# Kernel optimization log

Hardware: AMD Instinct MI355X
Metric: run time of the kernel (lower is better)

The kernel has to match this reference:

```python
import jax, jax.numpy as jnp
import numpy as np

B, T, H, W = 1024, 10, 32, 32
D = H * W          # MoE token dim = image_width**2
HID = 2 * D        # MoE expert hidden size
E, K = 4, 1        # num_experts, top_k
N_MOE = 5          # transform, add, quad, cubic, fourth


def setup_inputs() -> dict:
    key = jax.random.key(0)
    ks = jax.random.split(key, 6)
    s = 0.02
    return {
        "input": jax.random.normal(ks[0], (B, T, 1, H, W), jnp.float32),
        "conv1_w": jax.random.normal(ks[1], (10, 1, 3, 3, 3), jnp.float32) * s,
        "conv1_b": jnp.zeros((10,), jnp.float32),
        "conv2_w": jax.random.normal(ks[2], (1, 10, T, 3, 3), jnp.float32) * s,
        "conv2_b": jnp.zeros((1,), jnp.float32),
        "w_gate": jax.random.normal(ks[3], (N_MOE, D, E), jnp.float32) * s,
        "w1": jax.random.normal(ks[4], (N_MOE, E, D, HID), jnp.float32) * s,
        "b1": jnp.zeros((N_MOE, E, HID), jnp.float32),
        "w2": jax.random.normal(ks[5], (N_MOE, E, HID, D), jnp.float32) * s,
        "b2": jnp.zeros((N_MOE, E, D), jnp.float32),
    }


def _conv3d(x, w, b, pad):
    y = jax.lax.conv_general_dilated(
        x, w, (1, 1, 1), pad, dimension_numbers=("NCDHW", "OIDHW", "NCDHW"))
    return y + b[None, :, None, None, None]


def _cv_squared(x):
    eps = 1e-10
    return jnp.var(x, ddof=1) / (jnp.mean(x) ** 2 + eps)


def _moe(tok, wg, w1, b1, w2, b2):
    # tok: (B, D). Eval-mode noisy-top-k gating (clean logits, no noise).
    logits = tok @ wg                                   # (B, E)
    top_vals, top_idx = jax.lax.top_k(logits, K)
    top_g = jax.nn.softmax(top_vals, axis=1)            # k=1 -> gate == 1.0
    gates = jnp.zeros_like(logits).at[
        jnp.arange(tok.shape[0])[:, None], top_idx].set(top_g)
    # dense all-expert MLP (E=4 is small), combined by sparse gates
    h = jax.nn.relu(jnp.einsum("bd,edh->beh", tok, w1) + b1)
    y = jnp.einsum("beh,ehd->bed", h, w2) + b2
    out = jnp.einsum("be,bed->bd", gates, y)
    importance = gates.sum(0)
    load = (gates > 0).astype(tok.dtype).sum(0)
    loss = (_cv_squared(importance) + _cv_squared(load)) * 1e-2
    return out, loss


def reference(input, conv1_w, conv1_b, conv2_w, conv2_b, w_gate, w1, b1, w2, b2):
    x = jnp.transpose(input, (0, 2, 1, 3, 4))           # (B,1,T,H,W)
    x = jax.nn.relu(_conv3d(x, conv1_w, conv1_b, [(1, 1), (1, 1), (1, 1)]))
    x = jax.nn.relu(_conv3d(x, conv2_w, conv2_b, [(0, 0), (1, 1), (1, 1)]))  # (B,1,1,H,W)
    tok = x.reshape(x.shape[0], -1)                     # (B, D)
    outs, losses = jax.vmap(_moe, in_axes=(None, 0, 0, 0, 0, 0))(
        tok, w_gate, w1, b1, w2, b2)                    # (5,B,D), (5,)
    f = outs.reshape(N_MOE, -1, 1, 1, H, W)             # each broadcasts over T
    transform, add, quad, cubic, fourth = f[0], f[1], f[2], f[3], f[4]
    i2 = input * input
    poly = (i2 * i2 * fourth + i2 * input * cubic + i2 * quad
            + input * transform + add)
    out = jax.nn.sigmoid(poly)                          # encoder/decoder = identity
    return out, jnp.sum(losses)
```

## Files before the change

### kernel.cpp

```cpp
#include <hip/hip_runtime.h>
#include <hip/hip_bf16.h>


typedef __bf16 bf16x8 __attribute__((ext_vector_type(8)));
typedef __bf16 bf16x4 __attribute__((ext_vector_type(4)));
typedef __bf16 bf16x2 __attribute__((ext_vector_type(2)));
typedef float f32x4 __attribute__((ext_vector_type(4)));

#define NMOE 5
#define NEXP 4

__global__ __launch_bounds__(256, 3) void conv_tok_kernel(
    const float* __restrict__ input, const float* __restrict__ c1w,
    const float* __restrict__ c1b, const float* __restrict__ c2w,
    const float* __restrict__ c2b, float* __restrict__ tok_f32,
    __bf16* __restrict__ tok_bf16)
{
    __shared__ float in_s[10][34][34];
    __shared__ float P[34][34];
    const int b = blockIdx.x, tid = threadIdx.x;

    float* ls = &in_s[0][0][0];
    for (int i = tid; i < 10 * 34 * 34; i += 256) ls[i] = 0.f;
    for (int i = tid; i < 34 * 34; i += 256) (&P[0][0])[i] = 0.f;
    __syncthreads();

    const float* ip = input + (size_t)b * 10240;
    for (int i = tid; i < 2560; i += 256) {
        int t = i >> 8, rem = i & 255;
        int h = rem >> 3, w4 = rem & 7;
        float4 v = ((const float4*)ip)[i];
        float* dst = &in_s[t][h + 1][w4 * 4 + 1];
        dst[0] = v.x; dst[1] = v.y; dst[2] = v.z; dst[3] = v.w;
    }
    __syncthreads();

    const int wcol = tid & 31;
    const int r0 = (tid >> 5) * 4;
    const float c2bias = c2b[0];
    float tk0 = c2bias, tk1 = c2bias, tk2 = c2bias, tk3 = c2bias;

    for (int c = 0; c < 10; ++c) {
        float w1l[27];
        #pragma unroll
        for (int i = 0; i < 27; ++i) w1l[i] = c1w[c * 27 + i];
        const float c1bias = c1b[c];

        float a0[10], a1[10], a2[10], a3[10];
        #pragma unroll
        for (int t = 0; t < 10; ++t) {
            a0[t] = c1bias; a1[t] = c1bias; a2[t] = c1bias; a3[t] = c1bias;
        }

        #pragma unroll
        for (int ts = 0; ts < 10; ++ts) {
            float p0[3], p1[3], p2[3], p3[3], p4[3], p5[3];
            #pragma unroll
            for (int dw = 0; dw < 3; ++dw) {
                p0[dw] = in_s[ts][r0 + 0][wcol + dw];
                p1[dw] = in_s[ts][r0 + 1][wcol + dw];
                p2[dw] = in_s[ts][r0 + 2][wcol + dw];
                p3[dw] = in_s[ts][r0 + 3][wcol + dw];
                p4[dw] = in_s[ts][r0 + 4][wcol + dw];
                p5[dw] = in_s[ts][r0 + 5][wcol + dw];
            }
            #pragma unroll
            for (int dt = 0; dt < 3; ++dt) {
                const int t = ts - dt + 1;
                if (t < 0 || t > 9) continue;
                #pragma unroll
                for (int dw = 0; dw < 3; ++dw) {
                    float u0 = w1l[dt * 9 + 0 + dw];
                    float u1 = w1l[dt * 9 + 3 + dw];
                    float u2 = w1l[dt * 9 + 6 + dw];
                    a0[t] += u0 * p0[dw] + u1 * p1[dw] + u2 * p2[dw];
                    a1[t] += u0 * p1[dw] + u1 * p2[dw] + u2 * p3[dw];
                    a2[t] += u0 * p2[dw] + u1 * p3[dw] + u2 * p4[dw];
                    a3[t] += u0 * p3[dw] + u1 * p4[dw] + u2 * p5[dw];
                }
            }
            if (ts >= 1) {
                const int td = ts - 1;
                __syncthreads();
                P[r0 + 1][wcol + 1] = fmaxf(a0[td], 0.f);
                P[r0 + 2][wcol + 1] = fmaxf(a1[td], 0.f);
                P[r0 + 3][wcol + 1] = fmaxf(a2[td], 0.f);
                P[r0 + 4][wcol + 1] = fmaxf(a3[td], 0.f);
                __syncthreads();
                const int wb = (c * 10 + td) * 9;
                #pragma unroll
                for (int dw = 0; dw < 3; ++dw) {
                    float q0 = P[r0 + 0][wcol + dw];
                    float q1 = P[r0 + 1][wcol + dw];
                    float q2 = P[r0 + 2][wcol + dw];
                    float q3 = P[r0 + 3][wcol + dw];
                    float q4 = P[r0 + 4][wcol + dw];
                    float q5 = P[r0 + 5][wcol + dw];
                    float u0 = c2w[wb + 0 + dw];
                    float u1 = c2w[wb + 3 + dw];
                    float u2 = c2w[wb + 6 + dw];
                    tk0 += u0 * q0 + u1 * q1 + u2 * q2;
                    tk1 += u0 * q1 + u1 * q2 + u2 * q3;
                    tk2 += u0 * q2 + u1 * q3 + u2 * q4;
                    tk3 += u0 * q3 + u1 * q4 + u2 * q5;
                }
            }
        }
        {
            __syncthreads();
            P[r0 + 1][wcol + 1] = fmaxf(a0[9], 0.f);
            P[r0 + 2][wcol + 1] = fmaxf(a1[9], 0.f);
            P[r0 + 3][wcol + 1] = fmaxf(a2[9], 0.f);
            P[r0 + 4][wcol + 1] = fmaxf(a3[9], 0.f);
            __syncthreads();
            const int wb = (c * 10 + 9) * 9;
            #pragma unroll
            for (int dw = 0; dw < 3; ++dw) {
                float q0 = P[r0 + 0][wcol + dw];
                float q1 = P[r0 + 1][wcol + dw];
                float q2 = P[r0 + 2][wcol + dw];
                float q3 = P[r0 + 3][wcol + dw];
                float q4 = P[r0 + 4][wcol + dw];
                float q5 = P[r0 + 5][wcol + dw];
                float u0 = c2w[wb + 0 + dw];
                float u1 = c2w[wb + 3 + dw];
                float u2 = c2w[wb + 6 + dw];
                tk0 += u0 * q0 + u1 * q1 + u2 * q2;
                tk1 += u0 * q1 + u1 * q2 + u2 * q3;
                tk2 += u0 * q2 + u1 * q3 + u2 * q4;
                tk3 += u0 * q3 + u1 * q4 + u2 * q5;
            }
        }
    }
    float o0 = fmaxf(tk0, 0.f), o1 = fmaxf(tk1, 0.f);
    float o2 = fmaxf(tk2, 0.f), o3 = fmaxf(tk3, 0.f);
    size_t base = (size_t)b * 1024 + (size_t)r0 * 32 + wcol;
    tok_f32[base] = o0; tok_f32[base + 32] = o1;
    tok_f32[base + 64] = o2; tok_f32[base + 96] = o3;
    tok_bf16[base] = (__bf16)o0; tok_bf16[base + 32] = (__bf16)o1;
    tok_bf16[base + 64] = (__bf16)o2; tok_bf16[base + 96] = (__bf16)o3;
}

__global__ __launch_bounds__(256) void gating_kernel(
    const float* __restrict__ tok, const float* __restrict__ w_gate,
    int* __restrict__ expert_id, int* __restrict__ counts)
{
    int gw = blockIdx.x * 4 + (threadIdx.x >> 6);
    int l = threadIdx.x & 63;
    int n = gw >> 10, b = gw & 1023;
    const float* trow = tok + (size_t)b * 1024;
    const float* wg = w_gate + (size_t)n * 4096;
    float a0 = 0.f, a1 = 0.f, a2 = 0.f, a3 = 0.f;
    #pragma unroll
    for (int i = 0; i < 16; ++i) {
        int d = i * 64 + l;
        float tv = trow[d];
        float4 g4 = *(const float4*)(wg + d * 4);
        a0 += tv * g4.x; a1 += tv * g4.y; a2 += tv * g4.z; a3 += tv * g4.w;
    }
    #pragma unroll
    for (int off = 32; off >= 1; off >>= 1) {
        a0 += __shfl_xor(a0, off);
        a1 += __shfl_xor(a1, off);
        a2 += __shfl_xor(a2, off);
        a3 += __shfl_xor(a3, off);
    }
    if (l == 0) {
        int e = 0; float best = a0;
        if (a1 > best) { best = a1; e = 1; }
        if (a2 > best) { best = a2; e = 2; }
        if (a3 > best) { best = a3; e = 3; }
        expert_id[n * 1024 + b] = e;
        atomicAdd(&counts[n * 4 + e], 1);
    }
}

__global__ __launch_bounds__(1024) void scatter_kernel(
    const int* __restrict__ expert_id, const int* __restrict__ counts,
    int* __restrict__ row_base, int* __restrict__ rows)
{
    __shared__ int cur[4];
    int n = blockIdx.x, tid = threadIdx.x;
    if (tid == 0) {
        int c0 = counts[n * 4 + 0], c1 = counts[n * 4 + 1], c2 = counts[n * 4 + 2];
        cur[0] = 0; cur[1] = c0; cur[2] = c0 + c1; cur[3] = c0 + c1 + c2;
        row_base[n * 4 + 0] = cur[0]; row_base[n * 4 + 1] = cur[1];
        row_base[n * 4 + 2] = cur[2]; row_base[n * 4 + 3] = cur[3];
    }
    __syncthreads();
    int e = expert_id[n * 1024 + tid];
    int pos = atomicAdd(&cur[e], 1);
    rows[n * 1024 + pos] = tid;
}

template <int K, int N, int BN, bool GATHER, bool RELU, bool OUTBF>
__global__ __launch_bounds__(512) void moe_gemm_kernel(
    const __bf16* __restrict__ Abase, const float* __restrict__ Bsrc,
    const float* __restrict__ bias, const int* __restrict__ rows_all,
    const int* __restrict__ counts_all, const int* __restrict__ rowbase_all,
    __bf16* __restrict__ outB, float* __restrict__ outF)
{
    constexpr int CQ  = BN / 4;
    constexpr int UB  = BN / 64;
    constexpr int NFR = BN / 32;

    const int gy = blockIdx.y;
    const int mod = gy >> 4, rem = gy & 15;
    const int e = rem >> 2, mt = rem & 3;
    const int grp = mod * 4 + e;
    const int cnt = counts_all[grp];
    const int row0 = mt * 256;
    if (row0 >= cnt) return;
    const int rbase = rowbase_all[grp];
    const int valid = min(256, cnt - row0);
    const int n0 = blockIdx.x * BN;
    const int* rows = rows_all + mod * 1024;

    __shared__ alignas(16) __bf16 As[256 * 64];
    __shared__ alignas(16) __bf16 Bs[BN * 64];

    const int tid = threadIdx.x;
    const int l = tid & 63, w = tid >> 6;
    const int wr = w >> 1, wc = w & 1;

    const __bf16* aptr[4];
    int woffA[4];
    const __bf16* abase2 = GATHER ? Abase : (Abase + (size_t)mod * 1024 * (size_t)K);
    #pragma unroll
    for (int i = 0; i < 4; ++i) {
        int flat = tid + i * 512;
        int rr = flat >> 3, cc = flat & 7;
        int ri = rbase + row0 + min(rr, valid - 1);
        int ga = GATHER ? rows[ri] : ri;
        aptr[i] = abase2 + (size_t)ga * K + cc * 8;
        woffA[i] = rr * 64 + ((cc ^ (rr & 7)) * 8);
    }
    const float* bp0 = Bsrc + (size_t)grp * K * N + n0;
    const float* bptr[UB][2];
    int boff[UB], bx[UB];
    #pragma unroll
    for (int i = 0; i < UB; ++i) {
        int u = tid + i * 512;
        int rp = u / CQ, cq = u % CQ;
        bptr[i][0] = bp0 + (size_t)(2 * rp) * N + 4 * cq;
        bptr[i][1] = bp0 + (size_t)(2 * rp + 1) * N + 4 * cq;
        boff[i] = (4 * cq) * 64 + ((rp & 3) << 1);
        bx[i] = (rp >> 2) ^ (4 * (cq & 1)) ^ ((cq >> 1) & 7);
    }

    f32x4 acc[4][NFR];
    f32x4 zero = {0.f, 0.f, 0.f, 0.f};
    #pragma unroll
    for (int mi = 0; mi < 4; ++mi)
        #pragma unroll
        for (int ni = 0; ni < NFR; ++ni) acc[mi][ni] = zero;

    bf16x8 av[4], avn[4];
    f32x4 bv[UB][2], bvn[UB][2];
    #pragma unroll
    for (int i = 0; i < 4; ++i) av[i] = *(const bf16x8*)aptr[i];
    #pragma unroll
    for (int i = 0; i < UB; ++i) {
        bv[i][0] = *(const f32x4*)bptr[i][0];
        bv[i][1] = *(const f32x4*)bptr[i][1];
    }

    for (int k0 = 0; k0 < K; k0 += 64) {
        __syncthreads();
        #pragma unroll
        for (int i = 0; i < 4; ++i) *(bf16x8*)(As + woffA[i]) = av[i];
        #pragma unroll
        for (int i = 0; i < UB; ++i) {
            #pragma unroll
            for (int qq = 0; qq < 4; ++qq) {
                bf16x2 val = {(__bf16)bv[i][0][qq], (__bf16)bv[i][1][qq]};
                *(bf16x2*)(Bs + boff[i] + qq * 64 + ((bx[i] ^ qq) << 3)) = val;
            }
        }
        if (k0 + 64 < K) {
            #pragma unroll
            for (int i = 0; i < 4; ++i) {
                aptr[i] += 64;
                avn[i] = *(const bf16x8*)aptr[i];
            }
            #pragma unroll
            for (int i = 0; i < UB; ++i) {
                bptr[i][0] += (size_t)64 * N;
                bptr[i][1] += (size_t)64 * N;
                bvn[i][0] = *(const f32x4*)bptr[i][0];
                bvn[i][1] = *(const f32x4*)bptr[i][1];
            }
        }
        __syncthreads();
        #pragma unroll
        for (int kk = 0; kk < 2; ++kk) {
            bf16x8 af[4], bfv[NFR];
            #pragma unroll
            for (int mi = 0; mi < 4; ++mi) {
                int row = wr * 64 + mi * 16 + (l & 15);
                int cc = (kk * 4 + (l >> 4)) ^ (row & 7);
                af[mi] = *(const bf16x8*)(As + row * 64 + cc * 8);
            }
            #pragma unroll
            for (int ni = 0; ni < NFR; ++ni) {
                int nrow = wc * (BN / 2) + ni * 16 + (l & 15);
                int gg = (nrow ^ (nrow >> 3)) & 7;
                int cc = (kk * 4 + (l >> 4)) ^ gg;
                bfv[ni] = *(const bf16x8*)(Bs + nrow * 64 + cc * 8);
            }
            #pragma unroll
            for (int mi = 0; mi < 4; ++mi)
                #pragma unroll
                for (int ni = 0; ni < NFR; ++ni)
                    acc[mi][ni] = __builtin_amdgcn_mfma_f32_16x16x32_bf16(
                        af[mi], bfv[ni], acc[mi][ni], 0, 0, 0);
        }
        #pragma unroll
        for (int i = 0; i < 4; ++i) av[i] = avn[i];
        #pragma unroll
        for (int i = 0; i < UB; ++i) {
            bv[i][0] = bvn[i][0];
            bv[i][1] = bvn[i][1];
        }
    }

    const int lrow = l >> 4, lcol = l & 15;
    #pragma unroll
    for (int ni = 0; ni < NFR; ++ni) {
        int col = n0 + wc * (BN / 2) + ni * 16 + lcol;
        float bval = bias[(size_t)grp * N + col];
        #pragma unroll
        for (int mi = 0; mi < 4; ++mi) {
            #pragma unroll
            for (int j = 0; j < 4; ++j) {
                int rt = wr * 64 + mi * 16 + lrow * 4 + j;
                if (rt < valid) {
                    float v = acc[mi][ni][j] + bval;
                    if (RELU) v = fmaxf(v, 0.f);
                    int crow = rbase + row0 + rt;
                    if (OUTBF) {
                        outB[((size_t)mod * 1024 + crow) * N + col] = (__bf16)v;
                    } else {
                        int tokid = rows[crow];
                        outF[((size_t)mod * 1024 + tokid) * N + col] = v;
                    }
                }
            }
        }
    }
}

__global__ __launch_bounds__(256) void poly_kernel(
    const float* __restrict__ input, const float* __restrict__ moe,
    float* __restrict__ out)
{
    const int b = blockIdx.x, tid = threadIdx.x;
    float4 f0 = *(const float4*)(moe + (size_t)(0 * 1024 + b) * 1024 + tid * 4);
    float4 f1 = *(const float4*)(moe + (size_t)(1 * 1024 + b) * 1024 + tid * 4);
    float4 f2 = *(const float4*)(moe + (size_t)(2 * 1024 + b) * 1024 + tid * 4);
    float4 f3 = *(const float4*)(moe + (size_t)(3 * 1024 + b) * 1024 + tid * 4);
    float4 f4 = *(const float4*)(moe + (size_t)(4 * 1024 + b) * 1024 + tid * 4);
    const float4* ipv = (const float4*)(input + (size_t)b * 10240);
    float4* opv = (float4*)(out + (size_t)b * 10240);
    #pragma unroll
    for (int t = 0; t < 10; ++t) {
        float4 x = ipv[t * 256 + tid];
        float4 r;
        {
            float i2 = x.x * x.x;
            float p = i2 * (i2 * f4.x + x.x * f3.x + f2.x) + x.x * f0.x + f1.x;
            r.x = 1.f / (1.f + __expf(-p));
        }
        {
            float i2 = x.y * x.y;
            float p = i2 * (i2 * f4.y + x.y * f3.y + f2.y) + x.y * f0.y + f1.y;
            r.y = 1.f / (1.f + __expf(-p));
        }
        {
            float i2 = x.z * x.z;
            float p = i2 * (i2 * f4.z + x.z * f3.z + f2.z) + x.z * f0.z + f1.z;
            r.z = 1.f / (1.f + __expf(-p));
        }
        {
            float i2 = x.w * x.w;
            float p = i2 * (i2 * f4.w + x.w * f3.w + f2.w) + x.w * f0.w + f1.w;
            r.w = 1.f / (1.f + __expf(-p));
        }
        opv[t * 256 + tid] = r;
    }
}

__global__ void loss_kernel(const int* __restrict__ counts, float* __restrict__ out_loss)
{
    if (threadIdx.x == 0 && blockIdx.x == 0) {
        float total = 0.f;
        for (int n = 0; n < NMOE; ++n) {
            const float m = 256.f;
            float var = 0.f;
            for (int e = 0; e < 4; ++e) {
                float d = (float)counts[n * 4 + e] - m;
                var += d * d;
            }
            var *= (1.f / 3.f);
            float cv2 = var / (m * m + 1e-10f);
            total += 2.f * cv2 * 1e-2f;
        }
        *out_loss = total;
    }
}

extern "C" void kernel_launch(void* const* d_in, const int* in_sizes, int n_in,
                              void* d_out, int out_size, void* d_ws, size_t ws_size,
                              hipStream_t stream)
{
    (void)in_sizes; (void)n_in; (void)out_size; (void)ws_size;
    const float* input = (const float*)d_in[0];
    const float* c1w   = (const float*)d_in[1];
    const float* c1b   = (const float*)d_in[2];
    const float* c2w   = (const float*)d_in[3];
    const float* c2b   = (const float*)d_in[4];
    const float* wgate = (const float*)d_in[5];
    const float* w1    = (const float*)d_in[6];
    const float* b1    = (const float*)d_in[7];
    const float* w2    = (const float*)d_in[8];
    const float* b2    = (const float*)d_in[9];
    float* out = (float*)d_out;

    char* ws = (char*)d_ws;
    float*  tok_f32   = (float*)(ws + 0);
    __bf16* tok_bf16  = (__bf16*)(ws + 4194304);
    __bf16* h         = (__bf16*)(ws + 6291456);
    float*  moe_out   = (float*)(ws + 27262976);
    int*    rows      = (int*)(ws + 48234496);
    int*    expert_id = (int*)(ws + 48254976);
    int*    counts    = (int*)(ws + 48275456);
    int*    row_base  = (int*)(ws + 48275536);

    hipMemsetAsync(counts, 0, NMOE * NEXP * sizeof(int), stream);

    conv_tok_kernel<<<1024, 256, 0, stream>>>(input, c1w, c1b, c2w, c2b, tok_f32, tok_bf16);
    gating_kernel<<<1280, 256, 0, stream>>>(tok_f32, wgate, expert_id, counts);
    scatter_kernel<<<5, 1024, 0, stream>>>(expert_id, counts, row_base, rows);

    moe_gemm_kernel<1024, 2048, 128, true, true, true><<<dim3(16, 80), 512, 0, stream>>>(
        tok_bf16, w1, b1, rows, counts, row_base, h, nullptr);
    moe_gemm_kernel<2048, 1024, 64, false, false, false><<<dim3(16, 80), 512, 0, stream>>>(
        h, w2, b2, rows, counts, row_base, nullptr, moe_out);

    poly_kernel<<<1024, 256, 0, stream>>>(input, moe_out, out);
    loss_kernel<<<1, 64, 0, stream>>>(counts, out + 10485760);
}
```

Measured before the change: 445.9 us.

## Register-cache input stencil in conv kernel with row-major 4-wide thread tiling

Reworks the fused conv kernel so each thread owns four horizontally adjacent outputs in one row instead of four vertically stacked ones. Each thread preloads its 3x6 input neighbourhood for all ten time steps into registers, using one small shared staging tile in place of a 10x34x34 shared buffer. The per-channel loop is reordered to compute one conv1 time slice at a time. The aim is fewer LDS reads, much less shared memory, and vector float4 loads and stores. In exchange it holds about 150 preloaded values per thread, so register pressure rises, and the occupancy hint drops from 3 to 2 blocks per SM.

```diff
diff --git a/kernel.cpp b/kernel.cpp
--- a/kernel.cpp
+++ b/kernel.cpp
@@ -10,33 +10,43 @@
 #define NMOE 5
 #define NEXP 4
 
-__global__ __launch_bounds__(256, 3) void conv_tok_kernel(
+__global__ __launch_bounds__(256, 2) void conv_tok_kernel(
     const float* __restrict__ input, const float* __restrict__ c1w,
     const float* __restrict__ c1b, const float* __restrict__ c2w,
     const float* __restrict__ c2b, float* __restrict__ tok_f32,
     __bf16* __restrict__ tok_bf16)
 {
-    __shared__ float in_s[10][34][34];
-    __shared__ float P[34][34];
+    __shared__ float S[34][36];
+    __shared__ float P[34][36];
     const int b = blockIdx.x, tid = threadIdx.x;
-
-    float* ls = &in_s[0][0][0];
-    for (int i = tid; i < 10 * 34 * 34; i += 256) ls[i] = 0.f;
-    for (int i = tid; i < 34 * 34; i += 256) (&P[0][0])[i] = 0.f;
+    const int r = tid >> 3;
+    const int c0 = (tid & 7) * 4;
+
+    for (int i = tid; i < 34 * 36; i += 256) {
+        (&S[0][0])[i] = 0.f;
+        (&P[0][0])[i] = 0.f;
+    }
     __syncthreads();
 
     const float* ip = input + (size_t)b * 10240;
-    for (int i = tid; i < 2560; i += 256) {
-        int t = i >> 8, rem = i & 255;
-        int h = rem >> 3, w4 = rem & 7;
-        float4 v = ((const float4*)ip)[i];
-        float* dst = &in_s[t][h + 1][w4 * 4 + 1];
-        dst[0] = v.x; dst[1] = v.y; dst[2] = v.z; dst[3] = v.w;
-    }
-    __syncthreads();
-
-    const int wcol = tid & 31;
-    const int r0 = (tid >> 5) * 4;
+    const int li = (c0 == 0) ? 32 : (c0 - 1);
+    const int ri = (c0 == 28) ? 33 : (c0 + 4);
+
+    f32x4 pq[10][3];
+    float pl[10][3], pr[10][3];
+    #pragma unroll
+    for (int ts = 0; ts < 10; ++ts) {
+        if (ts > 0) __syncthreads();
+        *(f32x4*)&S[r + 1][c0] = *(const f32x4*)(ip + ts * 1024 + tid * 4);
+        __syncthreads();
+        #pragma unroll
+        for (int i = 0; i < 3; ++i) {
+            pq[ts][i] = *(const f32x4*)&S[r + i][c0];
+            pl[ts][i] = S[r + i][li];
+            pr[ts][i] = S[r + i][ri];
+        }
+    }
+
     const float c2bias = c2b[0];
     float tk0 = c2bias, tk1 = c2bias, tk2 = c2bias, tk3 = c2bias;
 
@@ -46,99 +56,58 @@
         for (int i = 0; i < 27; ++i) w1l[i] = c1w[c * 27 + i];
         const float c1bias = c1b[c];
 
-        float a0[10], a1[10], a2[10], a3[10];
         #pragma unroll
         for (int t = 0; t < 10; ++t) {
-            a0[t] = c1bias; a1[t] = c1bias; a2[t] = c1bias; a3[t] = c1bias;
-        }
-
-        #pragma unroll
-        for (int ts = 0; ts < 10; ++ts) {
-            float p0[3], p1[3], p2[3], p3[3], p4[3], p5[3];
-            #pragma unroll
-            for (int dw = 0; dw < 3; ++dw) {
-                p0[dw] = in_s[ts][r0 + 0][wcol + dw];
-                p1[dw] = in_s[ts][r0 + 1][wcol + dw];
-                p2[dw] = in_s[ts][r0 + 2][wcol + dw];
-                p3[dw] = in_s[ts][r0 + 3][wcol + dw];
-                p4[dw] = in_s[ts][r0 + 4][wcol + dw];
-                p5[dw] = in_s[ts][r0 + 5][wcol + dw];
-            }
+            float a0 = c1bias, a1 = c1bias, a2 = c1bias, a3 = c1bias;
             #pragma unroll
             for (int dt = 0; dt < 3; ++dt) {
-                const int t = ts - dt + 1;
-                if (t < 0 || t > 9) continue;
+                const int ts = t + dt - 1;
+                if (ts < 0 || ts > 9) continue;
                 #pragma unroll
                 for (int dw = 0; dw < 3; ++dw) {
-                    float u0 = w1l[dt * 9 + 0 + dw];
-                    float u1 = w1l[dt * 9 + 3 + dw];
-                    float u2 = w1l[dt * 9 + 6 + dw];
-                    a0[t] += u0 * p0[dw] + u1 * p1[dw] + u2 * p2[dw];
-                    a1[t] += u0 * p1[dw] + u1 * p2[dw] + u2 * p3[dw];
-                    a2[t] += u0 * p2[dw] + u1 * p3[dw] + u2 * p4[dw];
-                    a3[t] += u0 * p3[dw] + u1 * p4[dw] + u2 * p5[dw];
+                    const float u0 = w1l[dt * 9 + 0 + dw];
+                    const float u1 = w1l[dt * 9 + 3 + dw];
+                    const float u2 = w1l[dt * 9 + 6 + dw];
+#define CV(i, cidx) ((cidx) < 0 ? pl[ts][i] : ((cidx) > 3 ? pr[ts][i] : pq[ts][i][(cidx)]))
+                    a0 += u0 * CV(0, dw - 1) + u1 * CV(1, dw - 1) + u2 * CV(2, dw - 1);
+                    a1 += u0 * CV(0, dw + 0) + u1 * CV(1, dw + 0) + u2 * CV(2, dw + 0);
+                    a2 += u0 * CV(0, dw + 1) + u1 * CV(1, dw + 1) + u2 * CV(2, dw + 1);
+                    a3 += u0 * CV(0, dw + 2) + u1 * CV(1, dw + 2) + u2 * CV(2, dw + 2);
+#undef CV
                 }
             }
-            if (ts >= 1) {
-                const int td = ts - 1;
-                __syncthreads();
-                P[r0 + 1][wcol + 1] = fmaxf(a0[td], 0.f);
-                P[r0 + 2][wcol + 1] = fmaxf(a1[td], 0.f);
-                P[r0 + 3][wcol + 1] = fmaxf(a2[td], 0.f);
-                P[r0 + 4][wcol + 1] = fmaxf(a3[td], 0.f);
-                __syncthreads();
-                const int wb = (c * 10 + td) * 9;
-                #pragma unroll
-                for (int dw = 0; dw < 3; ++dw) {
-                    float q0 = P[r0 + 0][wcol + dw];
-                    float q1 = P[r0 + 1][wcol + dw];
-                    float q2 = P[r0 + 2][wcol + dw];
-                    float q3 = P[r0 + 3][wcol + dw];
-                    float q4 = P[r0 + 4][wcol + dw];
-                    float q5 = P[r0 + 5][wcol + dw];
-                    float u0 = c2w[wb + 0 + dw];
-                    float u1 = c2w[wb + 3 + dw];
-                    float u2 = c2w[wb + 6 + dw];
-                    tk0 += u0 * q0 + u1 * q1 + u2 * q2;
-                    tk1 += u0 * q1 + u1 * q2 + u2 * q3;
-                    tk2 += u0 * q2 + u1 * q3 + u2 * q4;
-                    tk3 += u0 * q3 + u1 * q4 + u2 * q5;
-                }
-            }
-        }
-        {
             __syncthreads();
-            P[r0 + 1][wcol + 1] = fmaxf(a0[9], 0.f);
-            P[r0 + 2][wcol + 1] = fmaxf(a1[9], 0.f);
-            P[r0 + 3][wcol + 1] = fmaxf(a2[9], 0.f);
-            P[r0 + 4][wcol + 1] = fmaxf(a3[9], 0.f);
+            f32x4 o = {fmaxf(a0, 0.f), fmaxf(a1, 0.f), fmaxf(a2, 0.f), fmaxf(a3, 0.f)};
+            *(f32x4*)&P[r + 1][c0] = o;
             __syncthreads();
-            const int wb = (c * 10 + 9) * 9;
+            const int wb = (c * 10 + t) * 9;
+            f32x4 q[3]; float ql[3], qr[3];
+            #pragma unroll
+            for (int i = 0; i < 3; ++i) {
+                q[i] = *(const f32x4*)&P[r + i][c0];
+                ql[i] = P[r + i][li];
+                qr[i] = P[r + i][ri];
+            }
             #pragma unroll
             for (int dw = 0; dw < 3; ++dw) {
-                float q0 = P[r0 + 0][wcol + dw];
-                float q1 = P[r0 + 1][wcol + dw];
-                float q2 = P[r0 + 2][wcol + dw];
-                float q3 = P[r0 + 3][wcol + dw];
-                float q4 = P[r0 + 4][wcol + dw];
-                float q5 = P[r0 + 5][wcol + dw];
-                float u0 = c2w[wb + 0 + dw];
-                float u1 = c2w[wb + 3 + dw];
-                float u2 = c2w[wb + 6 + dw];
-                tk0 += u0 * q0 + u1 * q1 + u2 * q2;
-                tk1 += u0 * q1 + u1 * q2 + u2 * q3;
-                tk2 += u0 * q2 + u1 * q3 + u2 * q4;
-                tk3 += u0 * q3 + u1 * q4 + u2 * q5;
+                const float u0 = c2w[wb + 0 + dw];
+                const float u1 = c2w[wb + 3 + dw];
+                const float u2 = c2w[wb + 6 + dw];
+#define QV(i, cidx) ((cidx) < 0 ? ql[i] : ((cidx) > 3 ? qr[i] : q[i][(cidx)]))
+                tk0 += u0 * QV(0, dw - 1) + u1 * QV(1, dw - 1) + u2 * QV(2, dw - 1);
+                tk1 += u0 * QV(0, dw + 0) + u1 * QV(1, dw + 0) + u2 * QV(2, dw + 0);
+                tk2 += u0 * QV(0, dw + 1) + u1 * QV(1, dw + 1) + u2 * QV(2, dw + 1);
+                tk3 += u0 * QV(0, dw + 2) + u1 * QV(1, dw + 2) + u2 * QV(2, dw + 2);
+#undef QV
             }
         }
     }
     float o0 = fmaxf(tk0, 0.f), o1 = fmaxf(tk1, 0.f);
     float o2 = fmaxf(tk2, 0.f), o3 = fmaxf(tk3, 0.f);
-    size_t base = (size_t)b * 1024 + (size_t)r0 * 32 + wcol;
-    tok_f32[base] = o0; tok_f32[base + 32] = o1;
-    tok_f32[base + 64] = o2; tok_f32[base + 96] = o3;
-    tok_bf16[base] = (__bf16)o0; tok_bf16[base + 32] = (__bf16)o1;
-    tok_bf16[base + 64] = (__bf16)o2; tok_bf16[base + 96] = (__bf16)o3;
+    size_t base = (size_t)b * 1024 + (size_t)r * 32 + c0;
+    *(f32x4*)(tok_f32 + base) = f32x4{o0, o1, o2, o3};
+    bf16x4 ob = {(__bf16)o0, (__bf16)o1, (__bf16)o2, (__bf16)o3};
+    *(bf16x4*)(tok_bf16 + base) = ob;
 }
 
 __global__ __launch_bounds__(256) void gating_kernel(
```

Measured after the change: 1.664 ms. +273.3%, slower.
